# Kernel optimization log

Measured on AMD Instinct MI355X. Metric: run time of the kernel, lower is better.

The kernel has to match this reference:

```python
import jax, jax.numpy as jnp
import numpy as np

N_TOKEN = 1024
FFN_MULT = 4
B = 32
D = 1024
LN_EPS = 1e-5


def _layer_norm(x, gamma, beta):
    mu = jnp.mean(x, axis=-1, keepdims=True)
    var = jnp.var(x, axis=-1, keepdims=True)
    return (x - mu) * jax.lax.rsqrt(var + LN_EPS) * gamma + beta


def setup_inputs() -> dict:
    key = jax.random.key(0)
    ks = jax.random.split(key, 12)
    n, m = N_TOKEN, FFN_MULT * N_TOKEN
    s_in = 1.0 / np.sqrt(n)
    s_ff = 1.0 / np.sqrt(m)
    return {
        "Q": jax.random.normal(ks[0], (B, n), jnp.float32),
        "K": jax.random.normal(ks[1], (B, n, D), jnp.float32),
        "V": jax.random.normal(ks[2], (B, n, D), jnp.float32),
        "mu_w": jax.random.uniform(ks[3], (n, n), jnp.float32, -s_in, s_in),
        "mu_b": jax.random.uniform(ks[4], (n,), jnp.float32, -s_in, s_in),
        "sigma_w": jax.random.uniform(ks[5], (n, n), jnp.float32, -s_in, s_in),
        "sigma_b": jax.random.uniform(ks[6], (n,), jnp.float32, -s_in, s_in),
        "ffn_w1": jax.random.uniform(ks[7], (m, n), jnp.float32, -s_in, s_in),
        "ffn_b1": jax.random.uniform(ks[8], (m,), jnp.float32, -s_in, s_in),
        "ffn_w2": jax.random.uniform(ks[9], (n, m), jnp.float32, -s_ff, s_ff),
        "ffn_b2": jax.random.uniform(ks[10], (n,), jnp.float32, -s_ff, s_ff),
        "ln_ff_g": jnp.ones((n,), jnp.float32),
        "ln_ff_b": jnp.zeros((n,), jnp.float32),
        "ln_q_g": jnp.ones((n,), jnp.float32),
        "ln_q_b": jnp.zeros((n,), jnp.float32),
    }


def reference(Q, K, V, mu_w, mu_b, sigma_w, sigma_b, ffn_w1, ffn_b1,
              ffn_w2, ffn_b2, ln_ff_g, ln_ff_b, ln_q_g, ln_q_b):
    q = _layer_norm(Q, ln_q_g, ln_q_b)                       # (B, n)
    mu = jnp.tanh(q @ mu_w.T + mu_b)[..., None]              # (B, n, 1)
    sigma = (q @ sigma_w.T + sigma_b)[..., None]             # (B, n, 1)
    # Gaussian-kernel pseudo-attention: broadcast over D then reduce
    S = jnp.exp(-0.5 * (K - mu) ** 2 / (sigma ** 2 + 1e-8))  # (B, n, D)
    A = jnp.sum(S * V, axis=-1)                              # (B, n)
    x = A + Q
    h = _layer_norm(x, ln_ff_g, ln_ff_b)
    h = jax.nn.silu(h @ ffn_w1.T + ffn_b1) @ ffn_w2.T + ffn_b2
    return x + h
```

## Files before the change

kernel.cpp:

```cpp
#include <hip/hip_runtime.h>

#define N_TOK  1024
#define D_DIM  1024
#define M_FFN  4096

__device__ __forceinline__ float wave_reduce(float v) {
    #pragma unroll
    for (int off = 32; off > 0; off >>= 1) v += __shfl_xor(v, off);
    return v;
}

__global__ void ln_kernel(const float* __restrict__ X,
                          const float* __restrict__ gam,
                          const float* __restrict__ bet,
                          float* __restrict__ Y) {
    int b = blockIdx.x, t = threadIdx.x;
    float4 x = ((const float4*)(X + (size_t)b * N_TOK))[t];
    float s = x.x + x.y + x.z + x.w;
    float q = x.x*x.x + x.y*x.y + x.z*x.z + x.w*x.w;
    s = wave_reduce(s); q = wave_reduce(q);
    __shared__ float sa[4], sb[4];
    int wid = t >> 6;
    if ((t & 63) == 0) { sa[wid] = s; sb[wid] = q; }
    __syncthreads();
    float ts = sa[0] + sa[1] + sa[2] + sa[3];
    float tq = sb[0] + sb[1] + sb[2] + sb[3];
    float mean = ts * (1.f / N_TOK);
    float var  = tq * (1.f / N_TOK) - mean * mean;
    float rs = rsqrtf(var + 1e-5f);
    float4 g4 = ((const float4*)gam)[t];
    float4 b4 = ((const float4*)bet)[t];
    float4 o;
    o.x = (x.x - mean) * rs * g4.x + b4.x;
    o.y = (x.y - mean) * rs * g4.y + b4.y;
    o.z = (x.z - mean) * rs * g4.z + b4.z;
    o.w = (x.w - mean) * rs * g4.w + b4.w;
    ((float4*)(Y + (size_t)b * N_TOK))[t] = o;
}

__global__ void gemm_kernel(const float* __restrict__ A,
                            const float* __restrict__ W0,
                            const float* __restrict__ W1,
                            float* __restrict__ C0,
                            float* __restrict__ C1,
                            const float* __restrict__ bias,
                            int N, int K, int kchunk, int mode) {
    int t = threadIdx.x;
    int lane = t & 63, wid = t >> 6;
    int ksub = lane & 15, nsub = lane >> 4;
    int mhalf = wid & 1, ngrp = wid >> 1;
    int n = blockIdx.x * 8 + ngrp * 4 + nsub;
    int k0 = blockIdx.y * kchunk + ksub * 4;
    const float* W = blockIdx.z ? W1 : W0;
    float*       C = blockIdx.z ? C1 : C0;
    const float* wp = W + (size_t)n * K + k0;
    const float* ap = A + (size_t)mhalf * 16 * K + k0;
    float acc[16];
    #pragma unroll
    for (int j = 0; j < 16; j++) acc[j] = 0.f;
    for (int kk = 0; kk < kchunk; kk += 64) {
        float4 w4 = *(const float4*)(wp + kk);
        #pragma unroll
        for (int j = 0; j < 16; j++) {
            float4 a4 = *(const float4*)(ap + (size_t)j * K + kk);
            acc[j] += a4.x*w4.x + a4.y*w4.y + a4.z*w4.z + a4.w*w4.w;
        }
    }
    #pragma unroll
    for (int j = 0; j < 16; j++) {
        #pragma unroll
        for (int off = 1; off < 16; off <<= 1)
            acc[j] += __shfl_xor(acc[j], off);
    }
    if (ksub == 0) {
        int mbase = mhalf * 16;
        if (mode == 2) {
            #pragma unroll
            for (int j = 0; j < 16; j++)
                atomicAdd(C + (size_t)(mbase + j) * N + n, acc[j]);
        } else if (mode == 1) {
            float bn = bias[n];
            #pragma unroll
            for (int j = 0; j < 16; j++) {
                float z = acc[j] + bn;
                C[(size_t)(mbase + j) * N + n] = z / (1.f + __expf(-z));
            }
        } else {
            #pragma unroll
            for (int j = 0; j < 16; j++)
                C[(size_t)(mbase + j) * N + n] = acc[j];
        }
    }
}

__global__ void attn_kernel(const float* __restrict__ Kp,
                            const float* __restrict__ Vp,
                            const float* __restrict__ Qp,
                            const float* __restrict__ mu_acc,
                            const float* __restrict__ sg_acc,
                            const float* __restrict__ mu_b,
                            const float* __restrict__ sg_b,
                            float* __restrict__ xo) {
    int t = threadIdx.x;
    int lane = t & 63, wid = t >> 6;
    int row0 = blockIdx.x * 16 + wid * 4;
    float4 ck[4], cv[4], nk[4], nv[4];
    {
        const float4* kp = (const float4*)(Kp + (size_t)row0 * D_DIM);
        const float4* vp = (const float4*)(Vp + (size_t)row0 * D_DIM);
        #pragma unroll
        for (int c = 0; c < 4; c++) { ck[c] = kp[c * 64 + lane]; cv[c] = vp[c * 64 + lane]; }
    }
    #pragma unroll
    for (int r = 0; r < 4; r++) {
        int row = row0 + r;
        if (r < 3) {
            const float4* kp = (const float4*)(Kp + (size_t)(row + 1) * D_DIM);
            const float4* vp = (const float4*)(Vp + (size_t)(row + 1) * D_DIM);
            #pragma unroll
            for (int c = 0; c < 4; c++) { nk[c] = kp[c * 64 + lane]; nv[c] = vp[c * 64 + lane]; }
        }
        int i = row & (N_TOK - 1);
        float mu = tanhf(mu_acc[row] + mu_b[i]);
        float sg = sg_acc[row] + sg_b[i];
        float coef = -0.5f / (sg * sg + 1e-8f);
        float acc = 0.f;
        #pragma unroll
        for (int c = 0; c < 4; c++) {
            float d;
            d = ck[c].x - mu; acc += __expf(coef * d * d) * cv[c].x;
            d = ck[c].y - mu; acc += __expf(coef * d * d) * cv[c].y;
            d = ck[c].z - mu; acc += __expf(coef * d * d) * cv[c].z;
            d = ck[c].w - mu; acc += __expf(coef * d * d) * cv[c].w;
        }
        acc = wave_reduce(acc);
        if (lane == 0) xo[row] = acc + Qp[row];
        if (r < 3) {
            #pragma unroll
            for (int c = 0; c < 4; c++) { ck[c] = nk[c]; cv[c] = nv[c]; }
        }
    }
}

__global__ void final_kernel(const float* __restrict__ x,
                             const float* __restrict__ acc2,
                             const float* __restrict__ b2,
                             float* __restrict__ out) {
    int idx = blockIdx.x * 256 + threadIdx.x;
    out[idx] = x[idx] + acc2[idx] + b2[idx & (N_TOK - 1)];
}

extern "C" void kernel_launch(void* const* d_in, const int* in_sizes, int n_in,
                              void* d_out, int out_size, void* d_ws, size_t ws_size,
                              hipStream_t stream) {
    const float* Q       = (const float*)d_in[0];
    const float* Kp      = (const float*)d_in[1];
    const float* Vp      = (const float*)d_in[2];
    const float* mu_w    = (const float*)d_in[3];
    const float* mu_b    = (const float*)d_in[4];
    const float* sigma_w = (const float*)d_in[5];
    const float* sigma_b = (const float*)d_in[6];
    const float* w1      = (const float*)d_in[7];
    const float* b1      = (const float*)d_in[8];
    const float* w2      = (const float*)d_in[9];
    const float* b2      = (const float*)d_in[10];
    const float* ln_ff_g = (const float*)d_in[11];
    const float* ln_ff_b = (const float*)d_in[12];
    const float* ln_q_g  = (const float*)d_in[13];
    const float* ln_q_b  = (const float*)d_in[14];

    float* mu_acc = (float*)d_ws;
    float* sg_acc = mu_acc + 32768;
    float* f2_acc = sg_acc + 32768;
    float* xbuf   = f2_acc + 32768;
    float* qln    = xbuf   + 32768;
    float* h0     = qln    + 32768;
    float* g      = h0     + 32768;

    hipMemsetAsync(f2_acc, 0, (size_t)32768 * sizeof(float), stream);

    ln_kernel<<<32, 256, 0, stream>>>(Q, ln_q_g, ln_q_b, qln);

    gemm_kernel<<<dim3(128, 1, 2), 256, 0, stream>>>(
        qln, mu_w, sigma_w, mu_acc, sg_acc, nullptr, 1024, 1024, 1024, 0);

    attn_kernel<<<2048, 256, 0, stream>>>(Kp, Vp, Q, mu_acc, sg_acc,
                                          mu_b, sigma_b, xbuf);

    ln_kernel<<<32, 256, 0, stream>>>(xbuf, ln_ff_g, ln_ff_b, h0);

    gemm_kernel<<<dim3(512, 1, 1), 256, 0, stream>>>(
        h0, w1, w1, g, g, b1, 4096, 1024, 1024, 1);

    gemm_kernel<<<dim3(128, 2, 1), 256, 0, stream>>>(
        g, w2, w2, f2_acc, f2_acc, nullptr, 1024, 4096, 2048, 2);
    final_kernel<<<128, 256, 0, stream>>>(xbuf, f2_acc, b2, (float*)d_out);
}
```

Measured before the change: 420.1 us.

## Use nontemporal loads, specialize GEMM kernels, and restructure attention to two rows per block

Adds nontemporal loads for the streamed weight rows in the GEMMs and for the K/V rows in the attention kernel, since each of these is read only once. The generic GEMM becomes an inlined body with three specialized kernels, so the mode, sizes and chunk become compile-time constants. The attention kernel now processes two rows per 256-thread block, with each thread loading one float4 per row, instead of four rows per wave with register prefetch. This raises the grid to 16384 blocks, giving more parallelism for latency hiding, but adds a shared-memory reduction and a barrier per block.

```diff
diff --git a/kernel.cpp b/kernel.cpp
--- a/kernel.cpp
+++ b/kernel.cpp
@@ -3,6 +3,8 @@
 #define N_TOK  1024
 #define D_DIM  1024
 #define M_FFN  4096
+
+typedef float f32x4 __attribute__((ext_vector_type(4)));
 
 __device__ __forceinline__ float wave_reduce(float v) {
     #pragma unroll
@@ -38,28 +40,25 @@
     ((float4*)(Y + (size_t)b * N_TOK))[t] = o;
 }
 
-__global__ void gemm_kernel(const float* __restrict__ A,
-                            const float* __restrict__ W0,
-                            const float* __restrict__ W1,
-                            float* __restrict__ C0,
-                            float* __restrict__ C1,
-                            const float* __restrict__ bias,
-                            int N, int K, int kchunk, int mode) {
+__device__ __forceinline__ void gemm_body(const float* __restrict__ A,
+                                          const float* __restrict__ W,
+                                          float* __restrict__ C,
+                                          const float* __restrict__ bias,
+                                          int N, int K, int kchunk, int mode,
+                                          int bx, int by) {
     int t = threadIdx.x;
     int lane = t & 63, wid = t >> 6;
     int ksub = lane & 15, nsub = lane >> 4;
     int mhalf = wid & 1, ngrp = wid >> 1;
-    int n = blockIdx.x * 8 + ngrp * 4 + nsub;
-    int k0 = blockIdx.y * kchunk + ksub * 4;
-    const float* W = blockIdx.z ? W1 : W0;
-    float*       C = blockIdx.z ? C1 : C0;
+    int n = bx * 8 + ngrp * 4 + nsub;
+    int k0 = by * kchunk + ksub * 4;
     const float* wp = W + (size_t)n * K + k0;
     const float* ap = A + (size_t)mhalf * 16 * K + k0;
     float acc[16];
     #pragma unroll
     for (int j = 0; j < 16; j++) acc[j] = 0.f;
     for (int kk = 0; kk < kchunk; kk += 64) {
-        float4 w4 = *(const float4*)(wp + kk);
+        f32x4 w4 = __builtin_nontemporal_load((const f32x4*)(wp + kk));
         #pragma unroll
         for (int j = 0; j < 16; j++) {
             float4 a4 = *(const float4*)(ap + (size_t)j * K + kk);
@@ -93,6 +92,29 @@
     }
 }
 
+__global__ void gemm_mu_sigma(const float* __restrict__ A,
+                              const float* __restrict__ W0,
+                              const float* __restrict__ W1,
+                              float* __restrict__ C0,
+                              float* __restrict__ C1) {
+    const float* W = blockIdx.z ? W1 : W0;
+    float*       C = blockIdx.z ? C1 : C0;
+    gemm_body(A, W, C, nullptr, 1024, 1024, 1024, 0, blockIdx.x, 0);
+}
+
+__global__ void gemm_ffn1(const float* __restrict__ A,
+                          const float* __restrict__ W,
+                          float* __restrict__ C,
+                          const float* __restrict__ bias) {
+    gemm_body(A, W, C, bias, 4096, 1024, 1024, 1, blockIdx.x, 0);
+}
+
+__global__ void gemm_ffn2(const float* __restrict__ A,
+                          const float* __restrict__ W,
+                          float* __restrict__ C) {
+    gemm_body(A, W, C, nullptr, 1024, 4096, 2048, 2, blockIdx.x, blockIdx.y);
+}
+
 __global__ void attn_kernel(const float* __restrict__ Kp,
                             const float* __restrict__ Vp,
                             const float* __restrict__ Qp,
@@ -102,44 +124,37 @@
                             const float* __restrict__ sg_b,
                             float* __restrict__ xo) {
     int t = threadIdx.x;
-    int lane = t & 63, wid = t >> 6;
-    int row0 = blockIdx.x * 16 + wid * 4;
-    float4 ck[4], cv[4], nk[4], nv[4];
-    {
-        const float4* kp = (const float4*)(Kp + (size_t)row0 * D_DIM);
-        const float4* vp = (const float4*)(Vp + (size_t)row0 * D_DIM);
-        #pragma unroll
-        for (int c = 0; c < 4; c++) { ck[c] = kp[c * 64 + lane]; cv[c] = vp[c * 64 + lane]; }
-    }
-    #pragma unroll
-    for (int r = 0; r < 4; r++) {
-        int row = row0 + r;
-        if (r < 3) {
-            const float4* kp = (const float4*)(Kp + (size_t)(row + 1) * D_DIM);
-            const float4* vp = (const float4*)(Vp + (size_t)(row + 1) * D_DIM);
-            #pragma unroll
-            for (int c = 0; c < 4; c++) { nk[c] = kp[c * 64 + lane]; nv[c] = vp[c * 64 + lane]; }
-        }
-        int i = row & (N_TOK - 1);
-        float mu = tanhf(mu_acc[row] + mu_b[i]);
-        float sg = sg_acc[row] + sg_b[i];
-        float coef = -0.5f / (sg * sg + 1e-8f);
-        float acc = 0.f;
-        #pragma unroll
-        for (int c = 0; c < 4; c++) {
-            float d;
-            d = ck[c].x - mu; acc += __expf(coef * d * d) * cv[c].x;
-            d = ck[c].y - mu; acc += __expf(coef * d * d) * cv[c].y;
-            d = ck[c].z - mu; acc += __expf(coef * d * d) * cv[c].z;
-            d = ck[c].w - mu; acc += __expf(coef * d * d) * cv[c].w;
-        }
-        acc = wave_reduce(acc);
-        if (lane == 0) xo[row] = acc + Qp[row];
-        if (r < 3) {
-            #pragma unroll
-            for (int c = 0; c < 4; c++) { ck[c] = nk[c]; cv[c] = nv[c]; }
-        }
-    }
+    int rowa = blockIdx.x * 2;
+    int rowb = rowa + 1;
+    const f32x4* kp = (const f32x4*)(Kp + (size_t)rowa * D_DIM);
+    const f32x4* vp = (const f32x4*)(Vp + (size_t)rowa * D_DIM);
+    f32x4 kA = __builtin_nontemporal_load(kp + t);
+    f32x4 kB = __builtin_nontemporal_load(kp + 256 + t);
+    f32x4 vA = __builtin_nontemporal_load(vp + t);
+    f32x4 vB = __builtin_nontemporal_load(vp + 256 + t);
+    int ia = rowa & (N_TOK - 1), ib = rowb & (N_TOK - 1);
+    float muA = tanhf(mu_acc[rowa] + mu_b[ia]);
+    float muB = tanhf(mu_acc[rowb] + mu_b[ib]);
+    float sgA = sg_acc[rowa] + sg_b[ia];
+    float sgB = sg_acc[rowb] + sg_b[ib];
+    float cA = -0.5f / (sgA * sgA + 1e-8f);
+    float cB = -0.5f / (sgB * sgB + 1e-8f);
+    float accA = 0.f, accB = 0.f, d;
+    d = kA.x - muA; accA += __expf(cA * d * d) * vA.x;
+    d = kA.y - muA; accA += __expf(cA * d * d) * vA.y;
+    d = kA.z - muA; accA += __expf(cA * d * d) * vA.z;
+    d = kA.w - muA; accA += __expf(cA * d * d) * vA.w;
+    d = kB.x - muB; accB += __expf(cB * d * d) * vB.x;
+    d = kB.y - muB; accB += __expf(cB * d * d) * vB.y;
+    d = kB.z - muB; accB += __expf(cB * d * d) * vB.z;
+    d = kB.w - muB; accB += __expf(cB * d * d) * vB.w;
+    accA = wave_reduce(accA); accB = wave_reduce(accB);
+    __shared__ float sA[4], sB[4];
+    int wid = t >> 6;
+    if ((t & 63) == 0) { sA[wid] = accA; sB[wid] = accB; }
+    __syncthreads();
+    if (t == 0)  xo[rowa] = sA[0] + sA[1] + sA[2] + sA[3] + Qp[rowa];
+    if (t == 64) xo[rowb] = sB[0] + sB[1] + sB[2] + sB[3] + Qp[rowb];
 }
 
 __global__ void final_kernel(const float* __restrict__ x,
@@ -181,18 +196,16 @@
 
     ln_kernel<<<32, 256, 0, stream>>>(Q, ln_q_g, ln_q_b, qln);
 
-    gemm_kernel<<<dim3(128, 1, 2), 256, 0, stream>>>(
-        qln, mu_w, sigma_w, mu_acc, sg_acc, nullptr, 1024, 1024, 1024, 0);
-
-    attn_kernel<<<2048, 256, 0, stream>>>(Kp, Vp, Q, mu_acc, sg_acc,
-                                          mu_b, sigma_b, xbuf);
+    gemm_mu_sigma<<<dim3(128, 1, 2), 256, 0, stream>>>(
+        qln, mu_w, sigma_w, mu_acc, sg_acc);
+
+    attn_kernel<<<16384, 256, 0, stream>>>(Kp, Vp, Q, mu_acc, sg_acc,
+                                           mu_b, sigma_b, xbuf);
 
     ln_kernel<<<32, 256, 0, stream>>>(xbuf, ln_ff_g, ln_ff_b, h0);
 
-    gemm_kernel<<<dim3(512, 1, 1), 256, 0, stream>>>(
-        h0, w1, w1, g, g, b1, 4096, 1024, 1024, 1);
-
-    gemm_kernel<<<dim3(128, 2, 1), 256, 0, stream>>>(
-        g, w2, w2, f2_acc, f2_acc, nullptr, 1024, 4096, 2048, 2);
+    gemm_ffn1<<<512, 256, 0, stream>>>(h0, w1, g, b1);
+
+    gemm_ffn2<<<dim3(128, 2), 256, 0, stream>>>(g, w2, f2_acc);
     final_kernel<<<128, 256, 0, stream>>>(xbuf, f2_acc, b2, (float*)d_out);
 }
```

Measured after the change: 398.4 us. -5.2%, faster.
